# Performance work log

Hardware: AMD Instinct MI355X
Metric: run time of the kernel (lower is better)

## Reference

```python
import jax, jax.numpy as jnp
import numpy as np

D_MODEL = 1024
NUM_HEADS = 16
THETA = 10000.0
NEG = -1000000.0  # masked_fill value used by the torch code


def _rope(x, token_positions, theta):
    # x: [B, H, S, d_head]; token_positions: [S] int
    d_k = x.shape[-1]
    half = d_k // 2
    j = jnp.arange(half, dtype=jnp.float32)
    inv_freq = theta ** (-(2.0 * j) / d_k)                      # [half]
    ang = token_positions.astype(jnp.float32)[:, None] * inv_freq  # [S, half]
    cos = jnp.cos(ang)
    sin = jnp.sin(ang)
    xp = x.reshape(x.shape[:-1] + (half, 2))  # adjacent pairs (pc, 2)
    x0, x1 = xp[..., 0], xp[..., 1]
    o0 = x0 * cos - x1 * sin
    o1 = x0 * sin + x1 * cos
    out = jnp.stack([o0, o1], axis=-1)
    return out.reshape(x.shape)


def setup_inputs() -> dict:
    key = jax.random.key(0)
    k0, k1, k2 = jax.random.split(key, 3)
    B, S, D = 2, 2048, D_MODEL
    std = (2.0 / (D + D)) ** 0.5
    X = jax.random.normal(k0, (B, S, D), dtype=jnp.float32)
    QKV_weights = jax.random.normal(k1, (3 * D, D), dtype=jnp.float32) * std
    O_weights = jax.random.normal(k2, (D, D), dtype=jnp.float32) * std
    token_positions = jnp.arange(S, dtype=jnp.int32)
    return {"X": X, "token_positions": token_positions,
            "QKV_weights": QKV_weights, "O_weights": O_weights}


def reference(X, token_positions, QKV_weights, O_weights):
    B, S, D = X.shape
    H = NUM_HEADS
    dh = D // H
    qkv = jnp.einsum('od,bsd->bso', QKV_weights, X)  # [B, S, 3D]
    Q, K, V = jnp.split(qkv, 3, axis=-1)

    def split_heads(t):
        return t.reshape(B, S, H, dh).transpose(0, 2, 1, 3)  # [B,H,S,dh]

    Q, K, V = split_heads(Q), split_heads(K), split_heads(V)
    Q = _rope(Q, token_positions, THETA)
    K = _rope(K, token_positions, THETA)

    scores = (jnp.einsum('bhqd,bhkd->bhqk', Q, K) / jnp.sqrt(jnp.float32(dh))).astype(jnp.float32)
    causal = jnp.tril(jnp.ones((S, S), dtype=bool))
    scores = jnp.where(causal, scores, NEG)
    probs = jax.nn.softmax(scores, axis=-1)
    attn = jnp.einsum('bhqk,bhkd->bhqd', probs, V.astype(jnp.float32)).astype(Q.dtype)
    attn = attn.transpose(0, 2, 1, 3).reshape(B, S, D)
    return jnp.einsum('od,bsd->bso', O_weights, attn)
```

## Files before the change

### kernel.cpp

```cpp
#include <hip/hip_runtime.h>
#include <math.h>

#define S_LEN 2048

using bf16x8  = __attribute__((ext_vector_type(8))) short;
using shortx4 = __attribute__((ext_vector_type(4))) short;
using f32x4   = __attribute__((ext_vector_type(4))) float;

static __device__ __forceinline__ short f2bf(float f) {
  unsigned u = __float_as_uint(f);
  u += 0x7fffu + ((u >> 16) & 1u);
  return (short)(u >> 16);
}
static __device__ __forceinline__ float bf2f(short s) {
  return __uint_as_float(((unsigned)(unsigned short)s) << 16);
}

#define GLD_LDS16(gptr, lptr)                                                  \
  __builtin_amdgcn_global_load_lds(                                            \
      (__attribute__((address_space(1))) void*)(gptr),                         \
      (__attribute__((address_space(3))) void*)(lptr), 16, 0, 0)

#define EXP2_SHIFT 20.0f

static __device__ __forceinline__ f32x4 exp2s4(f32x4 a) {
  return (f32x4){__builtin_amdgcn_exp2f(a[0] - EXP2_SHIFT),
                 __builtin_amdgcn_exp2f(a[1] - EXP2_SHIFT),
                 __builtin_amdgcn_exp2f(a[2] - EXP2_SHIFT),
                 __builtin_amdgcn_exp2f(a[3] - EXP2_SHIFT)};
}

static __device__ __forceinline__ int sigma64(int k) {
  return (k & 0x20) | ((k & 0x0C) << 1) | ((k & 0x10) >> 2) | (k & 3);
}

__global__ __launch_bounds__(256) void init_kernel(const float* __restrict__ X,
                                                   const float* __restrict__ W1,
                                                   const float* __restrict__ W2,
                                                   const int* __restrict__ tok,
                                                   short* __restrict__ Xb,
                                                   short* __restrict__ W1b,
                                                   short* __restrict__ W2b,
                                                   float2* __restrict__ table) {
  if (blockIdx.x < 4096) {
    size_t idx = (size_t)(blockIdx.x * 256 + threadIdx.x) * 8;
    const float* src;
    short* dst;
    size_t off;
    if (idx < 4194304) { src = X; dst = Xb; off = idx; }
    else if (idx < 4194304 + 3145728) { src = W1; dst = W1b; off = idx - 4194304; }
    else { src = W2; dst = W2b; off = idx - (4194304 + 3145728); }
    float4 a = *(const float4*)(src + off);
    float4 b = *(const float4*)(src + off + 4);
    bf16x8 o = {f2bf(a.x), f2bf(a.y), f2bf(a.z), f2bf(a.w),
                f2bf(b.x), f2bf(b.y), f2bf(b.z), f2bf(b.w)};
    *(bf16x8*)(dst + off) = o;
  } else {
    int i = (blockIdx.x - 4096) * 256 + threadIdx.x;
    int s = i >> 5, j = i & 31;
    double pos = (double)tok[s];
    double ang = pos * pow(10000.0, -(double)j / 32.0);
    table[i] = make_float2((float)cos(ang), (float)sin(ang));
  }
}

template <int BM, typename OutT>
__global__ __launch_bounds__(256) void gemm_ll(const short* __restrict__ A,
                                               const short* __restrict__ B,
                                               OutT* __restrict__ C,
                                               int M, int N, int K) {
  constexpr int MI = BM / 32;
  constexpr int AI = BM / 64;
  __shared__ short As[BM * 32];
  __shared__ short Bs[128 * 32];
  const int tid  = threadIdx.x;
  const int lane = tid & 63;
  const int wv   = tid >> 6;
  const int wm   = (wv >> 1) * (BM / 2);
  const int wn   = (wv & 1) * 64;
  const int m16  = lane & 15;
  const int q4   = lane >> 4;
  const int rowBase = blockIdx.y * BM;
  const int colBase = blockIdx.x * 128;
  const int lrow = lane >> 2;
  const int lchk = (lane & 3) ^ ((lane >> 3) & 3);
  const int fsw  = (q4 ^ ((m16 >> 1) & 3)) * 8;

  f32x4 acc[MI][4];
#pragma unroll
  for (int i = 0; i < MI; ++i)
#pragma unroll
    for (int j = 0; j < 4; ++j) acc[i][j] = (f32x4){0.f, 0.f, 0.f, 0.f};

  const short* Agl = A + (size_t)rowBase * K;
  const short* Bgl = B + (size_t)colBase * K;

  for (int kk = 0; kk < K; kk += 32) {
#pragma unroll
    for (int i = 0; i < AI; ++i) {
      const int r0 = (wv * AI + i) * 16;
      GLD_LDS16(Agl + (size_t)(r0 + lrow) * K + kk + lchk * 8, &As[r0 * 32]);
    }
#pragma unroll
    for (int i = 0; i < 2; ++i) {
      const int r0 = (wv * 2 + i) * 16;
      GLD_LDS16(Bgl + (size_t)(r0 + lrow) * K + kk + lchk * 8, &Bs[r0 * 32]);
    }
    __syncthreads();

    bf16x8 af[MI], bfv[4];
#pragma unroll
    for (int mi = 0; mi < MI; ++mi)
      af[mi] = *(const bf16x8*)&As[(wm + mi * 16 + m16) * 32 + fsw];
#pragma unroll
    for (int ni = 0; ni < 4; ++ni)
      bfv[ni] = *(const bf16x8*)&Bs[(wn + ni * 16 + m16) * 32 + fsw];
#pragma unroll
    for (int mi = 0; mi < MI; ++mi)
#pragma unroll
      for (int ni = 0; ni < 4; ++ni)
        acc[mi][ni] = __builtin_amdgcn_mfma_f32_16x16x32_bf16(af[mi], bfv[ni], acc[mi][ni], 0, 0, 0);
    __syncthreads();
  }

#pragma unroll
  for (int mi = 0; mi < MI; ++mi)
#pragma unroll
    for (int ni = 0; ni < 4; ++ni) {
      const int rbase = rowBase + wm + mi * 16 + q4 * 4;
      const int cidx  = colBase + wn + ni * 16 + m16;
#pragma unroll
      for (int r = 0; r < 4; ++r) {
        float v = acc[mi][ni][r];
        if constexpr (sizeof(OutT) == 2)
          C[(size_t)(rbase + r) * N + cidx] = (OutT)f2bf(v);
        else
          C[(size_t)(rbase + r) * N + cidx] = (OutT)v;
      }
    }
}

__global__ __launch_bounds__(256) void prep_kernel(const short* __restrict__ qkvb,
                                                   const float2* __restrict__ table,
                                                   short* __restrict__ Qb,
                                                   short* __restrict__ Kb,
                                                   short* __restrict__ VT) {
  __shared__ __align__(16) short VtL[64 * 72];
  const int tid = threadIdx.x;
  const int st  = blockIdx.x, bh = blockIdx.y;
  const int b   = bh >> 4, h = bh & 15;
  const int r   = tid >> 2, seg = tid & 3;
  const int s   = st * 64 + r;
  const int pr  = sigma64(r);
  const short* base = qkvb + (size_t)(b * S_LEN + s) * 3072 + h * 64 + seg * 16;
  const float QSCALE = 0.125f * 1.44269504f;

#pragma unroll
  for (int which = 0; which < 2; ++which) {
    const short* src = base + which * 1024;
    short in[16], ob[16];
    *(bf16x8*)&in[0] = ((const bf16x8*)src)[0];
    *(bf16x8*)&in[8] = ((const bf16x8*)src)[1];
#pragma unroll
    for (int p = 0; p < 8; ++p) {
      float x0 = bf2f(in[2 * p]), x1 = bf2f(in[2 * p + 1]);
      float2 cs = table[s * 32 + seg * 8 + p];
      float o0 = x0 * cs.x - x1 * cs.y;
      float o1 = x0 * cs.y + x1 * cs.x;
      if (which == 0) { o0 *= QSCALE; o1 *= QSCALE; }
      ob[2 * p]     = f2bf(o0);
      ob[2 * p + 1] = f2bf(o1);
    }
    short* dst = (which ? Kb : Qb) + ((size_t)bh * S_LEN + s) * 64 + seg * 16;
    ((bf16x8*)dst)[0] = *(bf16x8*)&ob[0];
    ((bf16x8*)dst)[1] = *(bf16x8*)&ob[8];
  }

  {
    const short* vsrc = base + 2048;
    short in[16];
    *(bf16x8*)&in[0] = ((const bf16x8*)vsrc)[0];
    *(bf16x8*)&in[8] = ((const bf16x8*)vsrc)[1];
#pragma unroll
    for (int d = 0; d < 16; ++d)
      VtL[(seg * 16 + d) * 72 + pr] = in[d];
  }
  __syncthreads();
  short* vdst = VT + ((size_t)bh * 64 + r) * S_LEN + st * 64 + seg * 16;
  ((bf16x8*)vdst)[0] = *(bf16x8*)&VtL[r * 72 + seg * 16];
  ((bf16x8*)vdst)[1] = *(bf16x8*)&VtL[r * 72 + seg * 16 + 8];
}

__global__ __launch_bounds__(256, 2) void attn_mfma(const short* __restrict__ Qb,
                                                    const short* __restrict__ Kb,
                                                    const short* __restrict__ VT,
                                                    short* __restrict__ attnb) {
  __shared__ __align__(16) short Smem[9216];
  short* Ks = Smem;
  short* Vs = Smem + 64 * 72;
  const int tid  = threadIdx.x;
  const int lane = tid & 63;
  const int w    = tid >> 6;
  const int m16  = lane & 15;
  const int q4   = lane >> 4;
  const int bh   = blockIdx.x;
  const int jtx  = blockIdx.y;
  const int jt   = (jtx < 8) ? (15 - jtx) : (jtx - 8);
  const int b    = bh >> 4, h = bh & 15;
  const short* Qh = Qb + (size_t)bh * S_LEN * 64;
  const short* Kh = Kb + (size_t)bh * S_LEN * 64;
  const short* Vh = VT + (size_t)bh * 64 * S_LEN;

  const int srow = tid >> 3;
  const int seg  = tid & 7;

  const bf16x8 ones = {16256, 16256, 16256, 16256, 16256, 16256, 16256, 16256};

  const int q0 = jt * 128;
  const int ktiles = 2 * jt + 2;

  bf16x8 qf[2][2];
#pragma unroll
  for (int n = 0; n < 2; ++n)
#pragma unroll
    for (int ks = 0; ks < 2; ++ks)
      qf[n][ks] = *(const bf16x8*)(Qh + (size_t)(q0 + w * 32 + n * 16 + m16) * 64 + ks * 32 + q4 * 8);

  f32x4 O[2][4], Lacc[2];
#pragma unroll
  for (int n = 0; n < 2; ++n) {
    Lacc[n] = (f32x4){0.f, 0.f, 0.f, 0.f};
#pragma unroll
    for (int c = 0; c < 4; ++c) O[n][c] = (f32x4){0.f, 0.f, 0.f, 0.f};
  }

  bf16x8 kst[2], vst[2];
#pragma unroll
  for (int i = 0; i < 2; ++i) {
    kst[i] = *(const bf16x8*)(Kh + (size_t)(i * 32 + srow) * 64 + seg * 8);
    vst[i] = *(const bf16x8*)(Vh + (size_t)(i * 32 + srow) * S_LEN + seg * 8);
  }

  for (int t = 0; t < ktiles; ++t) {
#pragma unroll
    for (int i = 0; i < 2; ++i) {
      *(bf16x8*)&Ks[(i * 32 + srow) * 72 + seg * 8] = kst[i];
      *(bf16x8*)&Vs[(i * 32 + srow) * 72 + seg * 8] = vst[i];
    }
    __syncthreads();

    if (t + 1 < ktiles) {
#pragma unroll
      for (int i = 0; i < 2; ++i) {
        kst[i] = *(const bf16x8*)(Kh + (size_t)((t + 1) * 64 + i * 32 + srow) * 64 + seg * 8);
        vst[i] = *(const bf16x8*)(Vh + (size_t)(i * 32 + srow) * S_LEN + (t + 1) * 64 + seg * 8);
      }
    }

    f32x4 sc[2][4];
#pragma unroll
    for (int n = 0; n < 2; ++n)
#pragma unroll
      for (int c = 0; c < 4; ++c) sc[n][c] = (f32x4){0.f, 0.f, 0.f, 0.f};
#pragma unroll
    for (int ks = 0; ks < 2; ++ks) {
#pragma unroll
      for (int c = 0; c < 4; ++c) {
        bf16x8 kf = *(const bf16x8*)&Ks[(c * 16 + m16) * 72 + ks * 32 + q4 * 8];
#pragma unroll
        for (int n = 0; n < 2; ++n)
          sc[n][c] = __builtin_amdgcn_mfma_f32_16x16x32_bf16(kf, qf[n][ks], sc[n][c], 0, 0, 0);
      }
    }

    if (t >= ktiles - 2) {
#pragma unroll
      for (int n = 0; n < 2; ++n)
#pragma unroll
        for (int c = 0; c < 4; ++c) {
          const int qg = q0 + w * 32 + n * 16 + m16;
#pragma unroll
          for (int rr = 0; rr < 4; ++rr) {
            const int kg = t * 64 + c * 16 + q4 * 4 + rr;
            if (kg > qg) sc[n][c][rr] = -1e30f;
          }
        }
    }

    bf16x8 pb[2][2];
#pragma unroll
    for (int n = 0; n < 2; ++n) {
#pragma unroll
      for (int c = 0; c < 4; ++c) sc[n][c] = exp2s4(sc[n][c]);
      pb[n][0] = (bf16x8){f2bf(sc[n][0][0]), f2bf(sc[n][0][1]), f2bf(sc[n][0][2]), f2bf(sc[n][0][3]),
                          f2bf(sc[n][1][0]), f2bf(sc[n][1][1]), f2bf(sc[n][1][2]), f2bf(sc[n][1][3])};
      pb[n][1] = (bf16x8){f2bf(sc[n][2][0]), f2bf(sc[n][2][1]), f2bf(sc[n][2][2]), f2bf(sc[n][2][3]),
                          f2bf(sc[n][3][0]), f2bf(sc[n][3][1]), f2bf(sc[n][3][2]), f2bf(sc[n][3][3])};
    }

#pragma unroll
    for (int ch = 0; ch < 2; ++ch) {
#pragma unroll
      for (int c2 = 0; c2 < 4; ++c2) {
        bf16x8 va = *(const bf16x8*)&Vs[(c2 * 16 + m16) * 72 + ch * 32 + q4 * 8];
#pragma unroll
        for (int n = 0; n < 2; ++n)
          O[n][c2] = __builtin_amdgcn_mfma_f32_16x16x32_bf16(va, pb[n][ch], O[n][c2], 0, 0, 0);
      }
#pragma unroll
      for (int n = 0; n < 2; ++n)
        Lacc[n] = __builtin_amdgcn_mfma_f32_16x16x32_bf16(ones, pb[n][ch], Lacc[n], 0, 0, 0);
    }
    __syncthreads();
  }

#pragma unroll
  for (int n = 0; n < 2; ++n) {
    const float inv = __frcp_rn(Lacc[n][0]);
#pragma unroll
    for (int c2 = 0; c2 < 4; ++c2) {
      shortx4 ov = {f2bf(O[n][c2][0] * inv), f2bf(O[n][c2][1] * inv),
                    f2bf(O[n][c2][2] * inv), f2bf(O[n][c2][3] * inv)};
      *(shortx4*)&Smem[(w * 32 + n * 16 + m16) * 72 + c2 * 16 + q4 * 4] = ov;
    }
  }
  __syncthreads();
  {
    const int row = tid >> 1, hf = tid & 1;
    const short* src = &Smem[row * 72 + hf * 32];
    short* dst = attnb + (size_t)(b * S_LEN + q0 + row) * 1024 + h * 64 + hf * 32;
    ((bf16x8*)dst)[0] = ((const bf16x8*)src)[0];
    ((bf16x8*)dst)[1] = ((const bf16x8*)src)[1];
    ((bf16x8*)dst)[2] = ((const bf16x8*)src)[2];
    ((bf16x8*)dst)[3] = ((const bf16x8*)src)[3];
  }
}

extern "C" void kernel_launch(void* const* d_in, const int* in_sizes, int n_in,
                              void* d_out, int out_size, void* d_ws, size_t ws_size,
                              hipStream_t stream) {
  const float* X    = (const float*)d_in[0];
  const int*   tok  = (const int*)d_in[1];
  const float* Wqkv = (const float*)d_in[2];
  const float* Wo   = (const float*)d_in[3];
  float* out = (float*)d_out;

  char* w = (char*)d_ws;
  float2* table = (float2*)w;
  short*  qkvb  = (short*)(w + 524288);
  short*  Qb    = (short*)(w + 524288 + 25165824);
  short*  Kb    = Qb + 4194304;
  short*  VTt   = Kb + 4194304;
  short*  Xb    = VTt + 4194304;
  short*  Wqkvb = Xb + 4194304;
  short*  Wob   = Wqkvb + 3145728;
  short*  attnb = qkvb;

  hipLaunchKernelGGL(init_kernel, dim3(4352), dim3(256), 0, stream,
                     X, Wqkv, Wo, tok, Xb, Wqkvb, Wob, table);
  hipLaunchKernelGGL((gemm_ll<128, short>), dim3(24, 32), dim3(256), 0, stream,
                     Xb, Wqkvb, qkvb, 4096, 3072, 1024);
  hipLaunchKernelGGL(prep_kernel, dim3(32, 32), dim3(256), 0, stream,
                     qkvb, table, Qb, Kb, VTt);
  hipLaunchKernelGGL(attn_mfma, dim3(32, 16), dim3(256), 0, stream,
                     Qb, Kb, VTt, attnb);
  hipLaunchKernelGGL((gemm_ll<64, float>), dim3(8, 64), dim3(256), 0, stream,
                     attnb, Wob, out, 4096, 1024, 1024);
}
```

Before: 184.0 us.

## Fuse RoPE and Q/K head split into QKV GEMM epilogue; packed bf16 converts

The QKV GEMM epilogue now applies RoPE (pairing adjacent columns with a lane shuffle), scales Q, and writes Q and K straight into per-head layout. V goes to a separate buffer, so the prep kernel shrinks to just the V transpose. This removes a full read and write of the Q and K intermediate. The attention kernel also switches to packed hardware bf16 conversion where available. The fused epilogue does scattered 2-byte stores and extra table loads, which may slow the GEMM tail.

```diff
diff --git a/kernel.cpp b/kernel.cpp
--- a/kernel.cpp
+++ b/kernel.cpp
@@ -6,15 +6,26 @@
 using bf16x8  = __attribute__((ext_vector_type(8))) short;
 using shortx4 = __attribute__((ext_vector_type(4))) short;
 using f32x4   = __attribute__((ext_vector_type(4))) float;
+using uintx4  = __attribute__((ext_vector_type(4))) unsigned;
+using uintx2  = __attribute__((ext_vector_type(2))) unsigned;
 
 static __device__ __forceinline__ short f2bf(float f) {
   unsigned u = __float_as_uint(f);
   u += 0x7fffu + ((u >> 16) & 1u);
   return (short)(u >> 16);
 }
-static __device__ __forceinline__ float bf2f(short s) {
-  return __uint_as_float(((unsigned)(unsigned short)s) << 16);
-}
+
+#if __has_builtin(__builtin_amdgcn_cvt_pk_bf16_f32)
+using bf16x2_t = __attribute__((ext_vector_type(2))) __bf16;
+static __device__ __forceinline__ unsigned pkbf(float a, float b) {
+  bf16x2_t v = __builtin_amdgcn_cvt_pk_bf16_f32(a, b);
+  return __builtin_bit_cast(unsigned, v);
+}
+#else
+static __device__ __forceinline__ unsigned pkbf(float a, float b) {
+  return (unsigned)(unsigned short)f2bf(a) | ((unsigned)(unsigned short)f2bf(b) << 16);
+}
+#endif
 
 #define GLD_LDS16(gptr, lptr)                                                  \
   __builtin_amdgcn_global_load_lds(                                            \
@@ -64,10 +75,14 @@
   }
 }
 
-template <int BM, typename OutT>
+template <int BM, typename OutT, int EPI>
 __global__ __launch_bounds__(256) void gemm_ll(const short* __restrict__ A,
                                                const short* __restrict__ B,
                                                OutT* __restrict__ C,
+                                               const float2* __restrict__ tab,
+                                               short* __restrict__ Qb,
+                                               short* __restrict__ Kb,
+                                               short* __restrict__ Vb,
                                                int M, int N, int K) {
   constexpr int MI = BM / 32;
   constexpr int AI = BM / 64;
@@ -123,28 +138,58 @@
     __syncthreads();
   }
 
-#pragma unroll
-  for (int mi = 0; mi < MI; ++mi)
-#pragma unroll
-    for (int ni = 0; ni < 4; ++ni) {
-      const int rbase = rowBase + wm + mi * 16 + q4 * 4;
-      const int cidx  = colBase + wn + ni * 16 + m16;
-#pragma unroll
-      for (int r = 0; r < 4; ++r) {
-        float v = acc[mi][ni][r];
-        if constexpr (sizeof(OutT) == 2)
-          C[(size_t)(rbase + r) * N + cidx] = (OutT)f2bf(v);
-        else
-          C[(size_t)(rbase + r) * N + cidx] = (OutT)v;
-      }
-    }
-}
-
-__global__ __launch_bounds__(256) void prep_kernel(const short* __restrict__ qkvb,
-                                                   const float2* __restrict__ table,
-                                                   short* __restrict__ Qb,
-                                                   short* __restrict__ Kb,
-                                                   short* __restrict__ VT) {
+  if constexpr (EPI == 0) {
+#pragma unroll
+    for (int mi = 0; mi < MI; ++mi)
+#pragma unroll
+      for (int ni = 0; ni < 4; ++ni) {
+        const int rbase = rowBase + wm + mi * 16 + q4 * 4;
+        const int cidx  = colBase + wn + ni * 16 + m16;
+#pragma unroll
+        for (int r = 0; r < 4; ++r) {
+          float v = acc[mi][ni][r];
+          if constexpr (sizeof(OutT) == 2)
+            C[(size_t)(rbase + r) * N + cidx] = (OutT)f2bf(v);
+          else
+            C[(size_t)(rbase + r) * N + cidx] = (OutT)v;
+        }
+      }
+  } else {
+    const int sect = colBase >> 10;
+#pragma unroll
+    for (int mi = 0; mi < MI; ++mi)
+#pragma unroll
+      for (int ni = 0; ni < 4; ++ni) {
+        const int col = colBase + wn + ni * 16 + m16;
+        const int rb  = rowBase + wm + mi * 16 + q4 * 4;
+        if (sect == 2) {
+          const int hd = col - 2048;
+#pragma unroll
+          for (int r = 0; r < 4; ++r)
+            Vb[(size_t)(rb + r) * 1024 + hd] = f2bf(acc[mi][ni][r]);
+        } else {
+          const int cc = col & 1023;
+          const int h = cc >> 6, d = cc & 63, j = d >> 1;
+          const float sgn = (m16 & 1) ? 1.f : -1.f;
+          short* dstp = (sect == 0) ? Qb : Kb;
+          const float scl = (sect == 0) ? (0.125f * 1.44269504f) : 1.f;
+#pragma unroll
+          for (int r = 0; r < 4; ++r) {
+            const int row = rb + r;
+            const int s = row & (S_LEN - 1), bidx = row >> 11;
+            float2 cs = tab[s * 32 + j];
+            float self = acc[mi][ni][r];
+            float part = __shfl_xor(self, 1);
+            float o = (self * cs.x + sgn * part * cs.y) * scl;
+            dstp[((size_t)((bidx * 16 + h) * S_LEN + s)) * 64 + d] = f2bf(o);
+          }
+        }
+      }
+  }
+}
+
+__global__ __launch_bounds__(256) void prep_v(const short* __restrict__ Vb,
+                                              short* __restrict__ VT) {
   __shared__ __align__(16) short VtL[64 * 72];
   const int tid = threadIdx.x;
   const int st  = blockIdx.x, bh = blockIdx.y;
@@ -152,32 +197,8 @@
   const int r   = tid >> 2, seg = tid & 3;
   const int s   = st * 64 + r;
   const int pr  = sigma64(r);
-  const short* base = qkvb + (size_t)(b * S_LEN + s) * 3072 + h * 64 + seg * 16;
-  const float QSCALE = 0.125f * 1.44269504f;
-
-#pragma unroll
-  for (int which = 0; which < 2; ++which) {
-    const short* src = base + which * 1024;
-    short in[16], ob[16];
-    *(bf16x8*)&in[0] = ((const bf16x8*)src)[0];
-    *(bf16x8*)&in[8] = ((const bf16x8*)src)[1];
-#pragma unroll
-    for (int p = 0; p < 8; ++p) {
-      float x0 = bf2f(in[2 * p]), x1 = bf2f(in[2 * p + 1]);
-      float2 cs = table[s * 32 + seg * 8 + p];
-      float o0 = x0 * cs.x - x1 * cs.y;
-      float o1 = x0 * cs.y + x1 * cs.x;
-      if (which == 0) { o0 *= QSCALE; o1 *= QSCALE; }
-      ob[2 * p]     = f2bf(o0);
-      ob[2 * p + 1] = f2bf(o1);
-    }
-    short* dst = (which ? Kb : Qb) + ((size_t)bh * S_LEN + s) * 64 + seg * 16;
-    ((bf16x8*)dst)[0] = *(bf16x8*)&ob[0];
-    ((bf16x8*)dst)[1] = *(bf16x8*)&ob[8];
-  }
-
   {
-    const short* vsrc = base + 2048;
+    const short* vsrc = Vb + (size_t)(b * S_LEN + s) * 1024 + h * 64 + seg * 16;
     short in[16];
     *(bf16x8*)&in[0] = ((const bf16x8*)vsrc)[0];
     *(bf16x8*)&in[8] = ((const bf16x8*)vsrc)[1];
@@ -292,10 +313,12 @@
     for (int n = 0; n < 2; ++n) {
 #pragma unroll
       for (int c = 0; c < 4; ++c) sc[n][c] = exp2s4(sc[n][c]);
-      pb[n][0] = (bf16x8){f2bf(sc[n][0][0]), f2bf(sc[n][0][1]), f2bf(sc[n][0][2]), f2bf(sc[n][0][3]),
-                          f2bf(sc[n][1][0]), f2bf(sc[n][1][1]), f2bf(sc[n][1][2]), f2bf(sc[n][1][3])};
-      pb[n][1] = (bf16x8){f2bf(sc[n][2][0]), f2bf(sc[n][2][1]), f2bf(sc[n][2][2]), f2bf(sc[n][2][3]),
-                          f2bf(sc[n][3][0]), f2bf(sc[n][3][1]), f2bf(sc[n][3][2]), f2bf(sc[n][3][3])};
+      uintx4 u0 = {pkbf(sc[n][0][0], sc[n][0][1]), pkbf(sc[n][0][2], sc[n][0][3]),
+                   pkbf(sc[n][1][0], sc[n][1][1]), pkbf(sc[n][1][2], sc[n][1][3])};
+      uintx4 u1 = {pkbf(sc[n][2][0], sc[n][2][1]), pkbf(sc[n][2][2], sc[n][2][3]),
+                   pkbf(sc[n][3][0], sc[n][3][1]), pkbf(sc[n][3][2], sc[n][3][3])};
+      pb[n][0] = __builtin_bit_cast(bf16x8, u0);
+      pb[n][1] = __builtin_bit_cast(bf16x8, u1);
     }
 
 #pragma unroll
@@ -319,9 +342,10 @@
     const float inv = __frcp_rn(Lacc[n][0]);
 #pragma unroll
     for (int c2 = 0; c2 < 4; ++c2) {
-      shortx4 ov = {f2bf(O[n][c2][0] * inv), f2bf(O[n][c2][1] * inv),
-                    f2bf(O[n][c2][2] * inv), f2bf(O[n][c2][3] * inv)};
-      *(shortx4*)&Smem[(w * 32 + n * 16 + m16) * 72 + c2 * 16 + q4 * 4] = ov;
+      uintx2 uo = {pkbf(O[n][c2][0] * inv, O[n][c2][1] * inv),
+                   pkbf(O[n][c2][2] * inv, O[n][c2][3] * inv)};
+      *(shortx4*)&Smem[(w * 32 + n * 16 + m16) * 72 + c2 * 16 + q4 * 4] =
+          __builtin_bit_cast(shortx4, uo);
     }
   }
   __syncthreads();
@@ -347,23 +371,24 @@
 
   char* w = (char*)d_ws;
   float2* table = (float2*)w;
-  short*  qkvb  = (short*)(w + 524288);
-  short*  Qb    = (short*)(w + 524288 + 25165824);
+  short*  Qb    = (short*)(w + 524288);
   short*  Kb    = Qb + 4194304;
   short*  VTt   = Kb + 4194304;
-  short*  Xb    = VTt + 4194304;
+  short*  Vb    = VTt + 4194304;
+  short*  Xb    = Vb + 4194304;
   short*  Wqkvb = Xb + 4194304;
   short*  Wob   = Wqkvb + 3145728;
-  short*  attnb = qkvb;
+  short*  attnb = Wob + 1048576;
 
   hipLaunchKernelGGL(init_kernel, dim3(4352), dim3(256), 0, stream,
                      X, Wqkv, Wo, tok, Xb, Wqkvb, Wob, table);
-  hipLaunchKernelGGL((gemm_ll<128, short>), dim3(24, 32), dim3(256), 0, stream,
-                     Xb, Wqkvb, qkvb, 4096, 3072, 1024);
-  hipLaunchKernelGGL(prep_kernel, dim3(32, 32), dim3(256), 0, stream,
-                     qkvb, table, Qb, Kb, VTt);
+  hipLaunchKernelGGL((gemm_ll<128, short, 1>), dim3(24, 32), dim3(256), 0, stream,
+                     Xb, Wqkvb, (short*)nullptr, table, Qb, Kb, Vb, 4096, 3072, 1024);
+  hipLaunchKernelGGL(prep_v, dim3(32, 32), dim3(256), 0, stream, Vb, VTt);
   hipLaunchKernelGGL(attn_mfma, dim3(32, 16), dim3(256), 0, stream,
                      Qb, Kb, VTt, attnb);
-  hipLaunchKernelGGL((gemm_ll<64, float>), dim3(8, 64), dim3(256), 0, stream,
-                     attnb, Wob, out, 4096, 1024, 1024);
-}
+  hipLaunchKernelGGL((gemm_ll<64, float, 0>), dim3(8, 64), dim3(256), 0, stream,
+                     attnb, Wob, out, (const float2*)nullptr,
+                     (short*)nullptr, (short*)nullptr, (short*)nullptr,
+                     4096, 1024, 1024);
+}
```

New measurement: 182.8 us. Within noise of the previous version (-0.7%).
